# Kernel optimization log

Hardware: AMD Instinct MI355X
Metric: run time of the kernel (lower is better)

The kernel has to match this reference:

```python
import jax, jax.numpy as jnp
import numpy as np

B, S, V, E, H = 64, 512, 32000, 256, 512


def setup_inputs() -> dict:
    key = jax.random.key(0)
    ks = jax.random.split(key, 8)
    s = 0.05
    return {
        "src": jax.random.randint(ks[0], (B, S), 0, V),
        "emb": jax.random.normal(ks[1], (V, E), dtype=jnp.float32) * s,
        "W_ih0": jax.random.normal(ks[2], (H, E), dtype=jnp.float32) * s,
        "W_hh0": jax.random.normal(ks[3], (H, H), dtype=jnp.float32) * s,
        "b_ih0": jnp.zeros((H,), jnp.float32),
        "b_hh0": jnp.zeros((H,), jnp.float32),
        "W_ih1": jax.random.normal(ks[4], (H, H), dtype=jnp.float32) * s,
        "W_hh1": jax.random.normal(ks[5], (H, H), dtype=jnp.float32) * s,
        "b_ih1": jnp.zeros((H,), jnp.float32),
        "b_hh1": jnp.zeros((H,), jnp.float32),
    }


def _rnn_layer(x, W_ih, W_hh, b_ih, b_hh):
    # x: [B,S,D] -> outputs [B,S,H], last hidden [B,H]
    # Precompute input projection for all timesteps (one big GEMM),
    # leaving only the h @ W_hh^T recurrence inside the scan.
    pre = jnp.einsum('bsd,hd->bsh', x, W_ih) + b_ih + b_hh  # [B,S,H]
    h0 = jnp.zeros((x.shape[0], W_hh.shape[0]), x.dtype)

    def step(h, p):
        h = jnp.tanh(p + h @ W_hh.T)
        return h, h

    hT, ys = jax.lax.scan(step, h0, jnp.swapaxes(pre, 0, 1))  # scan over time
    return jnp.swapaxes(ys, 0, 1), hT


def reference(src, emb, W_ih0, W_hh0, b_ih0, b_hh0, W_ih1, W_hh1, b_ih1, b_hh1):
    # Embedding lookup; dropout is identity in eval mode (deterministic baseline).
    x = emb[src]  # [B,S,E]
    y0, h_last0 = _rnn_layer(x, W_ih0, W_hh0, b_ih0, b_hh0)
    # inter-layer dropout also identity in eval mode
    y1, h_last1 = _rnn_layer(y0, W_ih1, W_hh1, b_ih1, b_hh1)
    hidden = jnp.stack([h_last0, h_last1], axis=0)  # [num_layers, B, H]
    return y1, hidden
```

## Files before the change

kernel.cpp:

```cpp
#include <hip/hip_runtime.h>
#include <math.h>

#define BB 64
#define SS 512
#define EE 256
#define HH 512

typedef unsigned long long ull;

template <int K>
__global__ __launch_bounds__(256) void k_proj(const float* __restrict__ Ain,
                                              const int* __restrict__ src,
                                              const float* __restrict__ emb,
                                              const float* __restrict__ Wih,
                                              const float* __restrict__ b1,
                                              const float* __restrict__ b2,
                                              float* __restrict__ out) {
    __shared__ __align__(16) float As[16][68];
    __shared__ __align__(16) float Bs[16][68];
    int tid = threadIdx.x;
    int m0 = blockIdx.x * 64;
    int n0 = blockIdx.y * 64;
    int tx = tid & 15, ty = tid >> 4;
    int lr = tid >> 2;
    int lc = (tid & 3) * 4;

    const float* arow;
    if (src) arow = emb + (size_t)src[m0 + lr] * EE;
    else     arow = Ain + (size_t)(m0 + lr) * K;
    const float* brow = Wih + (size_t)(n0 + lr) * K;

    float acc[4][4] = {};

    for (int k0 = 0; k0 < K; k0 += 16) {
        float4 av = *(const float4*)(arow + k0 + lc);
        float4 bv = *(const float4*)(brow + k0 + lc);
        __syncthreads();
        As[lc + 0][lr] = av.x; As[lc + 1][lr] = av.y;
        As[lc + 2][lr] = av.z; As[lc + 3][lr] = av.w;
        Bs[lc + 0][lr] = bv.x; Bs[lc + 1][lr] = bv.y;
        Bs[lc + 2][lr] = bv.z; Bs[lc + 3][lr] = bv.w;
        __syncthreads();
#pragma unroll
        for (int k = 0; k < 16; ++k) {
            float4 a = *(const float4*)&As[k][ty * 4];
            float4 b = *(const float4*)&Bs[k][tx * 4];
            acc[0][0] += a.x * b.x; acc[0][1] += a.x * b.y;
            acc[0][2] += a.x * b.z; acc[0][3] += a.x * b.w;
            acc[1][0] += a.y * b.x; acc[1][1] += a.y * b.y;
            acc[1][2] += a.y * b.z; acc[1][3] += a.y * b.w;
            acc[2][0] += a.z * b.x; acc[2][1] += a.z * b.y;
            acc[2][2] += a.z * b.z; acc[2][3] += a.z * b.w;
            acc[3][0] += a.w * b.x; acc[3][1] += a.w * b.y;
            acc[3][2] += a.w * b.z; acc[3][3] += a.w * b.w;
        }
    }

    int n = n0 + tx * 4;
    float bx_ = b1[n + 0] + b2[n + 0];
    float by_ = b1[n + 1] + b2[n + 1];
    float bz_ = b1[n + 2] + b2[n + 2];
    float bw_ = b1[n + 3] + b2[n + 3];
#pragma unroll
    for (int i = 0; i < 4; ++i) {
        int m = m0 + ty * 4 + i;
        float4 o;
        o.x = acc[i][0] + bx_; o.y = acc[i][1] + by_;
        o.z = acc[i][2] + bz_; o.w = acc[i][3] + bw_;
        *(float4*)(out + (size_t)m * HH + n) = o;
    }
}

__device__ __forceinline__ void rec_phase9(
    int t, int bX, int grow, int r, int w, int kown, int wbase,
    const float* __restrict__ pre,
    const float4* wA, const float4* wI, const float4* wH, float bias1,
    ull* __restrict__ hp0, ull* __restrict__ hp1,
    float* __restrict__ h0s, float* __restrict__ h1s,
    float (*red)[3][64],
    float* __restrict__ y, float& h0last, float& h1last) {
    float pv = 0.f;
    if (w == 0 && t < SS) pv = pre[((size_t)bX * SS + t) * HH + grow];

    const ull* s0p = hp0 + (size_t)(t & 1) * BB * HH + (size_t)bX * HH + kown;
    const ull* s1p = hp1 + (size_t)(t & 1) * BB * HH + (size_t)bX * HH + kown;
    ull q0, q1;
    const unsigned tt = (unsigned)t;
    for (;;) {
        q0 = __hip_atomic_load(s0p, __ATOMIC_RELAXED, __HIP_MEMORY_SCOPE_AGENT);
        q1 = __hip_atomic_load(s1p, __ATOMIC_RELAXED, __HIP_MEMORY_SCOPE_AGENT);
        unsigned d = (((unsigned)(q0 >> 32)) ^ tt) | (((unsigned)(q1 >> 32)) ^ tt);
        if (d == 0) break;
    }
    h0s[kown] = __uint_as_float((unsigned)q0);
    h1s[kown] = __uint_as_float((unsigned)q1);
    asm volatile("" ::: "memory");

    const float4* x0 = (const float4*)&h0s[wbase];
    const float4* x1 = (const float4*)&h1s[wbase];
    float aa = 0.f, ai = 0.f, ah = 0.f;
#pragma unroll
    for (int i = 0; i < 16; ++i) {
        const float4 xv = x0[i];
        const float4 zv = x1[i];
        const float4 a4 = wA[i];
        const float4 i4 = wI[i];
        const float4 h4 = wH[i];
        aa = fmaf(a4.x, xv.x, aa); aa = fmaf(a4.y, xv.y, aa);
        aa = fmaf(a4.z, xv.z, aa); aa = fmaf(a4.w, xv.w, aa);
        ai = fmaf(i4.x, xv.x, ai); ai = fmaf(i4.y, xv.y, ai);
        ai = fmaf(i4.z, xv.z, ai); ai = fmaf(i4.w, xv.w, ai);
        ah = fmaf(h4.x, zv.x, ah); ah = fmaf(h4.y, zv.y, ah);
        ah = fmaf(h4.z, zv.z, ah); ah = fmaf(h4.w, zv.w, ah);
    }
    red[w][0][r] = aa; red[w][1][r] = ai; red[w][2][r] = ah;
    __syncthreads();

    if (w == 0) {
        if (t < SS) {
            float s0 = red[0][0][r] + red[1][0][r] + red[2][0][r] + red[3][0][r] +
                       red[4][0][r] + red[5][0][r] + red[6][0][r] + red[7][0][r];
            float h0v = tanhf(pv + s0);
            h0last = h0v;
            ull pk = ((ull)(unsigned)(t + 1) << 32) | (ull)__float_as_uint(h0v);
            __hip_atomic_store(&hp0[(size_t)((t + 1) & 1) * BB * HH + (size_t)bX * HH + grow],
                               pk, __ATOMIC_RELAXED, __HIP_MEMORY_SCOPE_AGENT);
        }
    } else if (w == 1) {
        float si = red[0][1][r] + red[1][1][r] + red[2][1][r] + red[3][1][r] +
                   red[4][1][r] + red[5][1][r] + red[6][1][r] + red[7][1][r];
        float sh = red[0][2][r] + red[1][2][r] + red[2][2][r] + red[3][2][r] +
                   red[4][2][r] + red[5][2][r] + red[6][2][r] + red[7][2][r];
        float h1v = tanhf(si + sh + bias1);
        h1last = h1v;
        y[((size_t)bX * SS + (t - 1)) * HH + grow] = h1v;
        if (t < SS) {
            ull pk = ((ull)(unsigned)(t + 1) << 32) | (ull)__float_as_uint(h1v);
            __hip_atomic_store(&hp1[(size_t)((t + 1) & 1) * BB * HH + (size_t)bX * HH + grow],
                               pk, __ATOMIC_RELAXED, __HIP_MEMORY_SCOPE_AGENT);
        }
    }
}

__global__ __launch_bounds__(512, 2) void k_rec9(
    const float* __restrict__ pre,
    const float* __restrict__ Whh0,
    const float* __restrict__ Wih1,
    const float* __restrict__ Whh1,
    const float* __restrict__ b_ih1,
    const float* __restrict__ b_hh1,
    float* __restrict__ y,
    float* __restrict__ hlast,
    ull* __restrict__ hp0,
    ull* __restrict__ hp1) {
    __shared__ __align__(16) float h0s[HH], h1s[HH];
    __shared__ __align__(16) float redA[8][3][64], redB[8][3][64];

    const int tid = threadIdx.x;
    const int r = tid & 63;
    const int w = tid >> 6;
    const int bid = blockIdx.x;
    const int g = bid & 7;
    const int c = bid >> 3;
    const int grow = g * 64 + r;
    const int kown = w * 64 + r;
    const int wbase = w * 64;
    const int bA = c * 2, bB = c * 2 + 1;

    float4 wA[16], wI[16], wH[16];
    {
        const float* pA = Whh0 + (size_t)grow * HH + wbase;
        const float* pI = Wih1 + (size_t)grow * HH + wbase;
        const float* pH = Whh1 + (size_t)grow * HH + wbase;
#pragma unroll
        for (int i = 0; i < 16; ++i) {
            wA[i] = *(const float4*)(pA + i * 4);
            wI[i] = *(const float4*)(pI + i * 4);
            wH[i] = *(const float4*)(pH + i * 4);
        }
    }

    float h0lA = 0.f, h0lB = 0.f, h1lA = 0.f, h1lB = 0.f, bias1 = 0.f;
    if (w == 0) {
        float pA0 = pre[(size_t)bA * SS * HH + grow];
        h0lA = tanhf(pA0);
        ull pk = (1ULL << 32) | (ull)__float_as_uint(h0lA);
        __hip_atomic_store(&hp0[(size_t)1 * BB * HH + (size_t)bA * HH + grow], pk,
                           __ATOMIC_RELAXED, __HIP_MEMORY_SCOPE_AGENT);
        float pB0 = pre[(size_t)bB * SS * HH + grow];
        h0lB = tanhf(pB0);
        pk = (1ULL << 32) | (ull)__float_as_uint(h0lB);
        __hip_atomic_store(&hp0[(size_t)1 * BB * HH + (size_t)bB * HH + grow], pk,
                           __ATOMIC_RELAXED, __HIP_MEMORY_SCOPE_AGENT);
    } else if (w == 1) {
        bias1 = b_ih1[grow] + b_hh1[grow];
        ull pk = (1ULL << 32);
        __hip_atomic_store(&hp1[(size_t)1 * BB * HH + (size_t)bA * HH + grow], pk,
                           __ATOMIC_RELAXED, __HIP_MEMORY_SCOPE_AGENT);
        __hip_atomic_store(&hp1[(size_t)1 * BB * HH + (size_t)bB * HH + grow], pk,
                           __ATOMIC_RELAXED, __HIP_MEMORY_SCOPE_AGENT);
    }

    for (int t = 1; t <= SS; ++t) {
        rec_phase9(t, bA, grow, r, w, kown, wbase, pre, wA, wI, wH, bias1,
                   hp0, hp1, h0s, h1s, redA, y, h0lA, h1lA);
        rec_phase9(t, bB, grow, r, w, kown, wbase, pre, wA, wI, wH, bias1,
                   hp0, hp1, h0s, h1s, redB, y, h0lB, h1lB);
    }

    if (w == 0) {
        hlast[(size_t)bA * HH + grow] = h0lA;
        hlast[(size_t)bB * HH + grow] = h0lB;
    } else if (w == 1) {
        hlast[(size_t)BB * HH + (size_t)bA * HH + grow] = h1lA;
        hlast[(size_t)BB * HH + (size_t)bB * HH + grow] = h1lB;
    }
}

extern "C" void kernel_launch(void* const* d_in, const int* in_sizes, int n_in,
                              void* d_out, int out_size, void* d_ws, size_t ws_size,
                              hipStream_t stream) {
    const int*   src   = (const int*)d_in[0];
    const float* emb   = (const float*)d_in[1];
    const float* W_ih0 = (const float*)d_in[2];
    const float* W_hh0 = (const float*)d_in[3];
    const float* b_ih0 = (const float*)d_in[4];
    const float* b_hh0 = (const float*)d_in[5];
    const float* W_ih1 = (const float*)d_in[6];
    const float* W_hh1 = (const float*)d_in[7];
    const float* b_ih1 = (const float*)d_in[8];
    const float* b_hh1 = (const float*)d_in[9];

    float* out   = (float*)d_out;
    float* y_out = out;
    float* hlast = out + (size_t)BB * SS * HH;

    float* ws  = (float*)d_ws;
    float* pre = ws;
    ull* hp0 = (ull*)(ws + (size_t)BB * SS * HH);
    ull* hp1 = hp0 + (size_t)2 * BB * HH;

    k_proj<EE><<<dim3(512, 8), 256, 0, stream>>>(nullptr, src, emb, W_ih0,
                                                 b_ih0, b_hh0, pre);
    k_rec9<<<256, 512, 0, stream>>>(pre, W_hh0, W_ih1, W_hh1, b_ih1, b_hh1,
                                    y_out, hlast, hp0, hp1);
}
```

Before: 1.598 ms.

## Prefetch next batch's hidden state and spread reduction across all warps

The spin-wait on the other batch's hidden state is moved to after this batch's dot products and before the barrier, so polling for the next phase overlaps the current phase's compute instead of sitting serially at its start. The final cross-warp reduction, previously done by warps 0 and 1 alone summing eight partials each, is split across all eight warps: groups of four lanes each add two partials and combine them with shuffles. Together these aim to shorten the per-timestep critical path of the persistent recurrent kernel. The cost is more complex indexing, and polling slightly earlier may add contention on the flag words.

Result: slower. 2.940 ms (+83.9%).

```diff
diff --git a/kernel.cpp b/kernel.cpp
--- a/kernel.cpp
+++ b/kernel.cpp
@@ -71,29 +71,37 @@
     }
 }
 
-__device__ __forceinline__ void rec_phase9(
-    int t, int bX, int grow, int r, int w, int kown, int wbase,
-    const float* __restrict__ pre,
-    const float4* wA, const float4* wI, const float4* wH, float bias1,
-    ull* __restrict__ hp0, ull* __restrict__ hp1,
-    float* __restrict__ h0s, float* __restrict__ h1s,
-    float (*red)[3][64],
-    float* __restrict__ y, float& h0last, float& h1last) {
-    float pv = 0.f;
-    if (w == 0 && t < SS) pv = pre[((size_t)bX * SS + t) * HH + grow];
-
-    const ull* s0p = hp0 + (size_t)(t & 1) * BB * HH + (size_t)bX * HH + kown;
-    const ull* s1p = hp1 + (size_t)(t & 1) * BB * HH + (size_t)bX * HH + kown;
-    ull q0, q1;
-    const unsigned tt = (unsigned)t;
+__device__ __forceinline__ void spin_poll(
+    const ull* __restrict__ hp0, const ull* __restrict__ hp1,
+    int slot, int bX, int kown, unsigned tt, ull& q0, ull& q1) {
+    const ull* s0p = hp0 + (size_t)slot * BB * HH + (size_t)bX * HH + kown;
+    const ull* s1p = hp1 + (size_t)slot * BB * HH + (size_t)bX * HH + kown;
     for (;;) {
         q0 = __hip_atomic_load(s0p, __ATOMIC_RELAXED, __HIP_MEMORY_SCOPE_AGENT);
         q1 = __hip_atomic_load(s1p, __ATOMIC_RELAXED, __HIP_MEMORY_SCOPE_AGENT);
         unsigned d = (((unsigned)(q0 >> 32)) ^ tt) | (((unsigned)(q1 >> 32)) ^ tt);
         if (d == 0) break;
     }
-    h0s[kown] = __uint_as_float((unsigned)q0);
-    h1s[kown] = __uint_as_float((unsigned)q1);
+}
+
+__device__ __forceinline__ void rec_phase10(
+    int t, int bX, int tN, int bN, bool doNext,
+    int r, int w, int kown, int wbase,
+    int idx, int p, int grow0, int grow1, float bias1,
+    const float* __restrict__ pre,
+    const float4* wA, const float4* wI, const float4* wH,
+    ull* __restrict__ hp0, ull* __restrict__ hp1,
+    float* __restrict__ h0s, float* __restrict__ h1s,
+    float (*red)[3][64],
+    ull& qc0, ull& qc1,
+    ull& qn0, ull& qn1,
+    float* __restrict__ y, float& h0last, float& h1last) {
+    float pv = 0.f;
+    if (p == 0 && idx < 8 && t < SS)
+        pv = pre[((size_t)bX * SS + t) * HH + grow0];
+
+    h0s[kown] = __uint_as_float((unsigned)qc0);
+    h1s[kown] = __uint_as_float((unsigned)qc1);
     asm volatile("" ::: "memory");
 
     const float4* x0 = (const float4*)&h0s[wbase];
@@ -114,35 +122,46 @@
         ah = fmaf(h4.z, zv.z, ah); ah = fmaf(h4.w, zv.w, ah);
     }
     red[w][0][r] = aa; red[w][1][r] = ai; red[w][2][r] = ah;
+
+    if (doNext)
+        spin_poll(hp0, hp1, tN & 1, bN, kown, (unsigned)tN, qn0, qn1);
+
     __syncthreads();
 
-    if (w == 0) {
+    if (idx < 8) {
         if (t < SS) {
-            float s0 = red[0][0][r] + red[1][0][r] + red[2][0][r] + red[3][0][r] +
-                       red[4][0][r] + red[5][0][r] + red[6][0][r] + red[7][0][r];
-            float h0v = tanhf(pv + s0);
-            h0last = h0v;
-            ull pk = ((ull)(unsigned)(t + 1) << 32) | (ull)__float_as_uint(h0v);
-            __hip_atomic_store(&hp0[(size_t)((t + 1) & 1) * BB * HH + (size_t)bX * HH + grow],
-                               pk, __ATOMIC_RELAXED, __HIP_MEMORY_SCOPE_AGENT);
-        }
-    } else if (w == 1) {
-        float si = red[0][1][r] + red[1][1][r] + red[2][1][r] + red[3][1][r] +
-                   red[4][1][r] + red[5][1][r] + red[6][1][r] + red[7][1][r];
-        float sh = red[0][2][r] + red[1][2][r] + red[2][2][r] + red[3][2][r] +
-                   red[4][2][r] + red[5][2][r] + red[6][2][r] + red[7][2][r];
-        float h1v = tanhf(si + sh + bias1);
-        h1last = h1v;
-        y[((size_t)bX * SS + (t - 1)) * HH + grow] = h1v;
-        if (t < SS) {
-            ull pk = ((ull)(unsigned)(t + 1) << 32) | (ull)__float_as_uint(h1v);
-            __hip_atomic_store(&hp1[(size_t)((t + 1) & 1) * BB * HH + (size_t)bX * HH + grow],
-                               pk, __ATOMIC_RELAXED, __HIP_MEMORY_SCOPE_AGENT);
-        }
-    }
-}
-
-__global__ __launch_bounds__(512, 2) void k_rec9(
+            const int R = (w << 3) + idx;
+            float s = red[2 * p][0][R] + red[2 * p + 1][0][R];
+            s += __shfl_xor(s, 1);
+            s += __shfl_xor(s, 2);
+            if (p == 0) {
+                float h0v = tanhf(pv + s);
+                h0last = h0v;
+                ull pk = ((ull)(unsigned)(t + 1) << 32) | (ull)__float_as_uint(h0v);
+                __hip_atomic_store(&hp0[(size_t)((t + 1) & 1) * BB * HH + (size_t)bX * HH + grow0],
+                                   pk, __ATOMIC_RELAXED, __HIP_MEMORY_SCOPE_AGENT);
+            }
+        }
+    } else {
+        const int R = (w << 3) + idx - 8;
+        float si = red[2 * p][1][R] + red[2 * p + 1][1][R] +
+                   red[2 * p][2][R] + red[2 * p + 1][2][R];
+        si += __shfl_xor(si, 1);
+        si += __shfl_xor(si, 2);
+        if (p == 0) {
+            float h1v = tanhf(si + bias1);
+            h1last = h1v;
+            y[((size_t)bX * SS + (t - 1)) * HH + grow1] = h1v;
+            if (t < SS) {
+                ull pk = ((ull)(unsigned)(t + 1) << 32) | (ull)__float_as_uint(h1v);
+                __hip_atomic_store(&hp1[(size_t)((t + 1) & 1) * BB * HH + (size_t)bX * HH + grow1],
+                                   pk, __ATOMIC_RELAXED, __HIP_MEMORY_SCOPE_AGENT);
+            }
+        }
+    }
+}
+
+__global__ __launch_bounds__(512, 2) void k_rec10(
     const float* __restrict__ pre,
     const float* __restrict__ Whh0,
     const float* __restrict__ Wih1,
@@ -167,6 +186,11 @@
     const int wbase = w * 64;
     const int bA = c * 2, bB = c * 2 + 1;
 
+    const int idx = r >> 2;
+    const int p = r & 3;
+    const int grow0 = g * 64 + (w << 3) + idx;
+    const int grow1 = g * 64 + (w << 3) + (idx - 8);
+
     float4 wA[16], wI[16], wH[16];
     {
         const float* pA = Whh0 + (size_t)grow * HH + wbase;
@@ -179,41 +203,51 @@
             wH[i] = *(const float4*)(pH + i * 4);
         }
     }
-
-    float h0lA = 0.f, h0lB = 0.f, h1lA = 0.f, h1lB = 0.f, bias1 = 0.f;
+    float bias1 = 0.f;
+    if (idx >= 8) bias1 = b_ih1[grow1] + b_hh1[grow1];
+
+    float h0lA = 0.f, h0lB = 0.f, h1lA = 0.f, h1lB = 0.f;
     if (w == 0) {
         float pA0 = pre[(size_t)bA * SS * HH + grow];
-        h0lA = tanhf(pA0);
-        ull pk = (1ULL << 32) | (ull)__float_as_uint(h0lA);
+        float v = tanhf(pA0);
+        ull pk = (1ULL << 32) | (ull)__float_as_uint(v);
         __hip_atomic_store(&hp0[(size_t)1 * BB * HH + (size_t)bA * HH + grow], pk,
                            __ATOMIC_RELAXED, __HIP_MEMORY_SCOPE_AGENT);
         float pB0 = pre[(size_t)bB * SS * HH + grow];
-        h0lB = tanhf(pB0);
-        pk = (1ULL << 32) | (ull)__float_as_uint(h0lB);
+        v = tanhf(pB0);
+        pk = (1ULL << 32) | (ull)__float_as_uint(v);
         __hip_atomic_store(&hp0[(size_t)1 * BB * HH + (size_t)bB * HH + grow], pk,
                            __ATOMIC_RELAXED, __HIP_MEMORY_SCOPE_AGENT);
     } else if (w == 1) {
-        bias1 = b_ih1[grow] + b_hh1[grow];
         ull pk = (1ULL << 32);
         __hip_atomic_store(&hp1[(size_t)1 * BB * HH + (size_t)bA * HH + grow], pk,
                            __ATOMIC_RELAXED, __HIP_MEMORY_SCOPE_AGENT);
         __hip_atomic_store(&hp1[(size_t)1 * BB * HH + (size_t)bB * HH + grow], pk,
                            __ATOMIC_RELAXED, __HIP_MEMORY_SCOPE_AGENT);
     }
+    if (p == 0 && idx < 8) {
+        h0lA = tanhf(pre[(size_t)bA * SS * HH + grow0]);
+        h0lB = tanhf(pre[(size_t)bB * SS * HH + grow0]);
+    }
+
+    ull qa0, qa1, qb0, qb1;
+    spin_poll(hp0, hp1, 1, bA, kown, 1u, qa0, qa1);
 
     for (int t = 1; t <= SS; ++t) {
-        rec_phase9(t, bA, grow, r, w, kown, wbase, pre, wA, wI, wH, bias1,
-                   hp0, hp1, h0s, h1s, redA, y, h0lA, h1lA);
-        rec_phase9(t, bB, grow, r, w, kown, wbase, pre, wA, wI, wH, bias1,
-                   hp0, hp1, h0s, h1s, redB, y, h0lB, h1lB);
-    }
-
-    if (w == 0) {
-        hlast[(size_t)bA * HH + grow] = h0lA;
-        hlast[(size_t)bB * HH + grow] = h0lB;
-    } else if (w == 1) {
-        hlast[(size_t)BB * HH + (size_t)bA * HH + grow] = h1lA;
-        hlast[(size_t)BB * HH + (size_t)bB * HH + grow] = h1lB;
+        rec_phase10(t, bA, t, bB, true, r, w, kown, wbase, idx, p,
+                    grow0, grow1, bias1, pre, wA, wI, wH, hp0, hp1,
+                    h0s, h1s, redA, qa0, qa1, qb0, qb1, y, h0lA, h1lA);
+        rec_phase10(t, bB, t + 1, bA, (t < SS), r, w, kown, wbase, idx, p,
+                    grow0, grow1, bias1, pre, wA, wI, wH, hp0, hp1,
+                    h0s, h1s, redB, qb0, qb1, qa0, qa1, y, h0lB, h1lB);
+    }
+
+    if (p == 0 && idx < 8) {
+        hlast[(size_t)bA * HH + grow0] = h0lA;
+        hlast[(size_t)bB * HH + grow0] = h0lB;
+    } else if (p == 0 && idx >= 8) {
+        hlast[(size_t)BB * HH + (size_t)bA * HH + grow1] = h1lA;
+        hlast[(size_t)BB * HH + (size_t)bB * HH + grow1] = h1lB;
     }
 }
 
@@ -242,6 +276,6 @@
 
     k_proj<EE><<<dim3(512, 8), 256, 0, stream>>>(nullptr, src, emb, W_ih0,
                                                  b_ih0, b_hh0, pre);
-    k_rec9<<<256, 512, 0, stream>>>(pre, W_hh0, W_ih1, W_hh1, b_ih1, b_hh1,
-                                    y_out, hlast, hp0, hp1);
-}
+    k_rec10<<<256, 512, 0, stream>>>(pre, W_hh0, W_ih1, W_hh1, b_ih1, b_hh1,
+                                     y_out, hlast, hp0, hp1);
+}
```
